# Optimization experiments

Hardware: AMD Instinct MI355X
Metric: run time of the kernel (lower is better)

The kernel has to match this reference:

```python
import jax, jax.numpy as jnp
import numpy as np

E = 8        # num experts
K = 2        # top-k
H = 1024     # hidden size
F = 3584     # intermediate (ffn) size
B, S = 1, 2048


def setup_inputs() -> dict:
    key = jax.random.key(0)
    ks = jax.random.split(key, 5)
    scale_h = 1.0 / np.sqrt(H)
    scale_f = 1.0 / np.sqrt(F)
    return {
        "hidden_states": jax.random.normal(ks[0], (B, S, H), jnp.float32),
        "gate_w": jax.random.normal(ks[1], (E, H), jnp.float32) * scale_h,  # Linear [out,in]
        "w1": jax.random.normal(ks[2], (E, F, H), jnp.float32) * scale_h,
        "w3": jax.random.normal(ks[3], (E, F, H), jnp.float32) * scale_h,
        "w2": jax.random.normal(ks[4], (E, H, F), jnp.float32) * scale_f,
    }


def reference(hidden_states, gate_w, w1, w3, w2):
    b, s, h = hidden_states.shape
    x = hidden_states.reshape(-1, h)                       # [T,H]
    T = x.shape[0]
    # Router: softmax over experts, top-k, renormalize
    router_logits = x @ gate_w.T                           # [T,E]
    routing_weights = jax.nn.softmax(router_logits.astype(jnp.float32), axis=-1)
    topk_w, topk_idx = jax.lax.top_k(routing_weights, K)   # [T,K]
    topk_w = topk_w / jnp.sum(topk_w, axis=-1, keepdims=True)
    # Per-token, per-expert combine weight (0 for unselected experts) --
    # matches the original mask-and-sum over all experts.
    tok = jnp.arange(T)
    expert_weights = jnp.zeros((T, E), jnp.float32).at[tok[:, None], topk_idx].add(topk_w)  # [T,E]
    # Dense per-expert SiLU-gated MLP over all tokens (as the reference loop does),
    # vectorized across experts.
    g = jnp.einsum("th,efh->etf", x, w1)                   # [E,T,F]
    u = jnp.einsum("th,efh->etf", x, w3)                   # [E,T,F]
    act = jax.nn.silu(g) * u                               # [E,T,F]
    y = jnp.einsum("etf,ehf->eth", act, w2)                # [E,T,H]
    out = jnp.einsum("eth,te->th", y, expert_weights.astype(y.dtype))  # [T,H]
    return out.reshape(b, s, h)
```

## Files before the change

kernel.cpp:

```cpp
#include <hip/hip_runtime.h>
#include <hip/hip_bf16.h>

#define T_TOK 2048
#define HID   1024
#define FF    3584
#define NE    8
#define TOPK  2
#define GRIDY 24

typedef __bf16 bf16x8 __attribute__((ext_vector_type(8)));
typedef float  f32x4  __attribute__((ext_vector_type(4)));

#define WS_COUNTS   0u
#define WS_OFFSETS  64u
#define WS_TILECNT  128u
#define WS_TLE      256u
#define WS_TLM      512u
#define WS_TOPKI    4096u
#define WS_TOPKW    20480u
#define WS_SLOTPOS  36864u
#define WS_SLOTROW  53248u
#define WS_ROUTETOK 69632u
#define WS_XG       131072u
#define WS_ACT      (WS_XG + 4096u*1024u*2u)
#define WS_Y        (WS_ACT + 4096u*3584u*2u)
#define Y_STRIDE    (4096u*1024u)

static __device__ __forceinline__ unsigned short f2bf(float f) {
    unsigned int u = __builtin_bit_cast(unsigned int, f);
    u += 0x7FFFu + ((u >> 16) & 1u);
    return (unsigned short)(u >> 16);
}
static __device__ __forceinline__ unsigned int pack2(float a, float b) {
    unsigned int ua = __builtin_bit_cast(unsigned int, a) + 0x8000u;
    unsigned int ub = __builtin_bit_cast(unsigned int, b) + 0x8000u;
    return (ua >> 16) | (ub & 0xFFFF0000u);
}
static __device__ __forceinline__ void gl_lds16(const void* g, void* l) {
    __builtin_amdgcn_global_load_lds((const __attribute__((address_space(1))) unsigned int*)g,
                                     (__attribute__((address_space(3))) unsigned int*)l, 16, 0, 0);
}

__global__ __launch_bounds__(256) void k_router(
    const float* __restrict__ x, const float* __restrict__ gw,
    int* __restrict__ counts, int* __restrict__ topki,
    float* __restrict__ topkw, int* __restrict__ slotpos)
{
    int t = blockIdx.x * 4 + (threadIdx.x >> 6);
    int l = threadIdx.x & 63;
    const float* xr = x + (size_t)t * HID;
    float acc[NE];
#pragma unroll
    for (int e = 0; e < NE; ++e) acc[e] = 0.f;
#pragma unroll
    for (int i = 0; i < 4; ++i) {
        int h = l * 4 + i * 256;
        float4 xv = *(const float4*)(xr + h);
#pragma unroll
        for (int e = 0; e < NE; ++e) {
            float4 g = *(const float4*)(gw + e * HID + h);
            acc[e] += xv.x * g.x + xv.y * g.y + xv.z * g.z + xv.w * g.w;
        }
    }
#pragma unroll
    for (int e = 0; e < NE; ++e) {
#pragma unroll
        for (int off = 32; off; off >>= 1) acc[e] += __shfl_xor(acc[e], off);
    }
    if (l == 0) {
        float best = -1e30f, second = -1e30f;
        int bi = 0, si = 0;
#pragma unroll
        for (int e = 0; e < NE; ++e) {
            float v = acc[e];
            if (v > best) { second = best; si = bi; best = v; bi = e; }
            else if (v > second) { second = v; si = e; }
        }
        float w0 = 1.f / (1.f + __expf(second - best));
        float w1 = 1.f - w0;
        topki[2 * t] = bi;  topki[2 * t + 1] = si;
        topkw[2 * t] = w0;  topkw[2 * t + 1] = w1;
        slotpos[2 * t]     = atomicAdd(&counts[bi], 1);
        slotpos[2 * t + 1] = atomicAdd(&counts[si], 1);
    }
}

__global__ void k_prefix(const int* __restrict__ counts, int* __restrict__ offsets,
                         int* __restrict__ tle, int* __restrict__ tlm,
                         int* __restrict__ tilecnt) {
    if (threadIdx.x == 0) {
        int o = 0;
#pragma unroll
        for (int e = 0; e < NE; ++e) { offsets[e] = o; o += counts[e]; }
        int n = 0;
        for (int e = 0; e < NE; ++e) {
            int t = (counts[e] + 255) >> 8;
            for (int i = 0; i < t; ++i) { tle[n] = e; tlm[n] = i; ++n; }
        }
        tilecnt[0] = n;
    }
}

__global__ void k_fill(const int* __restrict__ topki, const int* __restrict__ slotpos,
                       const int* __restrict__ offsets, int* __restrict__ routetok,
                       int* __restrict__ slotrow) {
    int j = blockIdx.x * blockDim.x + threadIdx.x;
    if (j >= T_TOK * TOPK) return;
    int e = topki[j];
    int row = offsets[e] + slotpos[j];
    routetok[row] = j >> 1;
    slotrow[j] = row;
}

__global__ void k_gather(const float* __restrict__ x, const int* __restrict__ routetok,
                         unsigned short* __restrict__ xg) {
    int j = blockIdx.x * blockDim.x + threadIdx.x;
    int r = j >> 8;
    int c = (j & 255) * 4;
    int tok = routetok[r];
    float4 v = *(const float4*)(x + (size_t)tok * HID + c);
    ushort4 o;
    o.x = f2bf(v.x); o.y = f2bf(v.y); o.z = f2bf(v.z); o.w = f2bf(v.w);
    int sc = c ^ ((r & 7) << 3);
    *(ushort4*)(xg + (size_t)r * HID + sc) = o;
}

__global__ __launch_bounds__(256, 2) void k_gemm1(
    const unsigned short* __restrict__ xg, const float* __restrict__ w1,
    const float* __restrict__ w3, const int* __restrict__ counts,
    const int* __restrict__ offsets, const int* __restrict__ tle,
    const int* __restrict__ tlm, const int* __restrict__ tilecnt,
    unsigned short* __restrict__ act)
{
    int by = blockIdx.y;
    if (by >= tilecnt[0]) return;
    int e = tle[by];
    int rbase = tlm[by] * 256;
    int cnt = counts[e], obase = offsets[e];
    int fbase = blockIdx.x * 64;

    __shared__ __align__(16) unsigned short lA[2][256 * 64];
    __shared__ __align__(16) unsigned short lB1[64 * 64];
    __shared__ __align__(16) unsigned short lB3[64 * 64];

    int tid = threadIdx.x;
    int lane = tid & 63, wv = tid >> 6;
    int wr = wv >> 1, wc = wv & 1;

    const unsigned short* asrc[8];
#pragma unroll
    for (int j = 0; j < 8; ++j) {
        int r = rbase + (tid >> 3) + 32 * j;
        int rg = obase + (r < cnt ? r : (cnt - 1));
        asrc[j] = xg + (size_t)rg * HID + (tid & 7) * 8;
    }
    unsigned short* adst = &lA[0][0] + tid * 8;

    int rb = tid & 63;
    int swzW = (rb & 7) << 3;
    const float* pb1 = w1 + ((size_t)e * FF + fbase + rb) * HID + wv * 16;
    const float* pb3 = w3 + ((size_t)e * FF + fbase + rb) * HID + wv * 16;
    unsigned short* wb1a = lB1 + rb * 64 + ((wv * 16) ^ swzW);
    unsigned short* wb1b = lB1 + rb * 64 + ((wv * 16 + 8) ^ swzW);
    unsigned short* wb3a = lB3 + rb * 64 + ((wv * 16) ^ swzW);
    unsigned short* wb3b = lB3 + rb * 64 + ((wv * 16 + 8) ^ swzW);

    int swzA = (((obase & 7) + (lane & 7)) & 7) << 3;
    int swzB = (lane & 7) << 3;
    int klane = (lane >> 4) * 8;

    f32x4 accg[8][2], accu[8][2];
#pragma unroll
    for (int m = 0; m < 8; ++m)
#pragma unroll
        for (int n = 0; n < 2; ++n) {
            accg[m][n] = (f32x4){0.f, 0.f, 0.f, 0.f};
            accu[m][n] = (f32x4){0.f, 0.f, 0.f, 0.f};
        }

#pragma unroll
    for (int j = 0; j < 8; ++j) gl_lds16(asrc[j], adst + 32 * j * 64);
    float4 r1[4], r3[4];
#pragma unroll
    for (int j = 0; j < 4; ++j) {
        r1[j] = *(const float4*)(pb1 + 4 * j);
        r3[j] = *(const float4*)(pb3 + 4 * j);
    }

    for (int kt = 0; kt < HID / 64; ++kt) {
        int cur = kt & 1;
        if (kt < HID / 64 - 1) {
            unsigned short* nd = &lA[cur ^ 1][0] + tid * 8;
#pragma unroll
            for (int j = 0; j < 8; ++j) gl_lds16(asrc[j] + (kt + 1) * 64, nd + 32 * j * 64);
        }
        {
            uint4 q;
            q.x = pack2(r1[0].x, r1[0].y); q.y = pack2(r1[0].z, r1[0].w);
            q.z = pack2(r1[1].x, r1[1].y); q.w = pack2(r1[1].z, r1[1].w);
            *(uint4*)wb1a = q;
            q.x = pack2(r1[2].x, r1[2].y); q.y = pack2(r1[2].z, r1[2].w);
            q.z = pack2(r1[3].x, r1[3].y); q.w = pack2(r1[3].z, r1[3].w);
            *(uint4*)wb1b = q;
            q.x = pack2(r3[0].x, r3[0].y); q.y = pack2(r3[0].z, r3[0].w);
            q.z = pack2(r3[1].x, r3[1].y); q.w = pack2(r3[1].z, r3[1].w);
            *(uint4*)wb3a = q;
            q.x = pack2(r3[2].x, r3[2].y); q.y = pack2(r3[2].z, r3[2].w);
            q.z = pack2(r3[3].x, r3[3].y); q.w = pack2(r3[3].z, r3[3].w);
            *(uint4*)wb3b = q;
        }
        if (kt < HID / 64 - 1) {
            int kof = (kt + 1) * 64;
#pragma unroll
            for (int j = 0; j < 4; ++j) {
                r1[j] = *(const float4*)(pb1 + kof + 4 * j);
                r3[j] = *(const float4*)(pb3 + kof + 4 * j);
            }
        }
        asm volatile("s_waitcnt lgkmcnt(0)" ::: "memory");
        __builtin_amdgcn_s_barrier();
        __builtin_amdgcn_sched_barrier(0);
        const unsigned short* A = &lA[cur][0];
#pragma unroll
        for (int kk = 0; kk < 2; ++kk) {
            int kc = kk * 32 + klane;
            int kA = kc ^ swzA, kB = kc ^ swzB;
            bf16x8 b1f[2], b3f[2];
#pragma unroll
            for (int n = 0; n < 2; ++n) {
                b1f[n] = *(const bf16x8*)(lB1 + (wc * 32 + n * 16 + (lane & 15)) * 64 + kB);
                b3f[n] = *(const bf16x8*)(lB3 + (wc * 32 + n * 16 + (lane & 15)) * 64 + kB);
            }
#pragma unroll
            for (int m = 0; m < 8; ++m) {
                bf16x8 a = *(const bf16x8*)(A + (wr * 128 + m * 16 + (lane & 15)) * 64 + kA);
#pragma unroll
                for (int n = 0; n < 2; ++n) {
                    accg[m][n] = __builtin_amdgcn_mfma_f32_16x16x32_bf16(a, b1f[n], accg[m][n], 0, 0, 0);
                    accu[m][n] = __builtin_amdgcn_mfma_f32_16x16x32_bf16(a, b3f[n], accu[m][n], 0, 0, 0);
                }
            }
        }
        __builtin_amdgcn_sched_barrier(0);
        asm volatile("s_waitcnt lgkmcnt(0)" ::: "memory");
        __builtin_amdgcn_s_barrier();
    }

#pragma unroll
    for (int m = 0; m < 8; ++m)
#pragma unroll
        for (int n = 0; n < 2; ++n)
#pragma unroll
            for (int r = 0; r < 4; ++r) {
                int lr = wr * 128 + m * 16 + (lane >> 4) * 4 + r;
                if (rbase + lr < cnt) {
                    float g = accg[m][n][r], u = accu[m][n][r];
                    float s = g / (1.f + __expf(-g));
                    int row = obase + rbase + lr;
                    int col = fbase + wc * 32 + n * 16 + (lane & 15);
                    int scol = col ^ ((row & 7) << 3);
                    act[(size_t)row * FF + scol] = f2bf(s * u);
                }
            }
}

__global__ __launch_bounds__(256, 2) void k_gemm2(
    const unsigned short* __restrict__ act, const float* __restrict__ w2,
    const int* __restrict__ counts, const int* __restrict__ offsets,
    const int* __restrict__ tle, const int* __restrict__ tlm,
    const int* __restrict__ tilecnt, float* __restrict__ y, int ks)
{
    int by = blockIdx.y;
    if (by >= tilecnt[0]) return;
    int e = tle[by];
    int rbase = tlm[by] * 256;
    int cnt = counts[e], obase = offsets[e];
    int hbase = blockIdx.x * 128;
    int z = blockIdx.z;
    const int KTOT = FF / 64;
    int per = (KTOT + ks - 1) / ks;
    int kt0 = z * per;
    int ktn = min(KTOT, kt0 + per) - kt0;

    __shared__ __align__(16) unsigned short lA[2][256 * 64];
    __shared__ __align__(16) unsigned short lB[128 * 64];

    int tid = threadIdx.x;
    int lane = tid & 63, wv = tid >> 6;
    int wr = wv >> 1, wc = wv & 1;

    const unsigned short* asrc[8];
#pragma unroll
    for (int j = 0; j < 8; ++j) {
        int r = rbase + (tid >> 3) + 32 * j;
        int rg = obase + (r < cnt ? r : (cnt - 1));
        asrc[j] = act + (size_t)rg * FF + kt0 * 64 + (tid & 7) * 8;
    }
    unsigned short* adst = &lA[0][0] + tid * 8;

    int hr = tid & 127, kh = tid >> 7;
    int swzW = (hr & 7) << 3;
    const float* pb = w2 + ((size_t)e * HID + hbase + hr) * FF + kt0 * 64 + kh * 32;
    unsigned short* wb[4];
#pragma unroll
    for (int j = 0; j < 4; ++j)
        wb[j] = lB + hr * 64 + ((kh * 32 + j * 8) ^ swzW);

    int swzA = (((obase & 7) + (lane & 7)) & 7) << 3;
    int swzB = (lane & 7) << 3;
    int klane = (lane >> 4) * 8;

    f32x4 acc[8][4];
#pragma unroll
    for (int m = 0; m < 8; ++m)
#pragma unroll
        for (int n = 0; n < 4; ++n) acc[m][n] = (f32x4){0.f, 0.f, 0.f, 0.f};

#pragma unroll
    for (int j = 0; j < 8; ++j) gl_lds16(asrc[j], adst + 32 * j * 64);
    float4 rw[8];
#pragma unroll
    for (int j = 0; j < 8; ++j) rw[j] = *(const float4*)(pb + 4 * j);

    for (int kt = 0; kt < ktn; ++kt) {
        int cur = kt & 1;
        if (kt < ktn - 1) {
            unsigned short* nd = &lA[cur ^ 1][0] + tid * 8;
#pragma unroll
            for (int j = 0; j < 8; ++j) gl_lds16(asrc[j] + (kt + 1) * 64, nd + 32 * j * 64);
        }
        {
            uint4 q;
#pragma unroll
            for (int j = 0; j < 4; ++j) {
                q.x = pack2(rw[2 * j].x, rw[2 * j].y);
                q.y = pack2(rw[2 * j].z, rw[2 * j].w);
                q.z = pack2(rw[2 * j + 1].x, rw[2 * j + 1].y);
                q.w = pack2(rw[2 * j + 1].z, rw[2 * j + 1].w);
                *(uint4*)wb[j] = q;
            }
        }
        if (kt < ktn - 1) {
            int kof = (kt + 1) * 64;
#pragma unroll
            for (int j = 0; j < 8; ++j) rw[j] = *(const float4*)(pb + kof + 4 * j);
        }
        asm volatile("s_waitcnt lgkmcnt(0)" ::: "memory");
        __builtin_amdgcn_s_barrier();
        __builtin_amdgcn_sched_barrier(0);
        const unsigned short* A = &lA[cur][0];
#pragma unroll
        for (int kk = 0; kk < 2; ++kk) {
            int kc = kk * 32 + klane;
            int kA = kc ^ swzA, kB = kc ^ swzB;
            bf16x8 bf[4];
#pragma unroll
            for (int n = 0; n < 4; ++n)
                bf[n] = *(const bf16x8*)(lB + (wc * 64 + n * 16 + (lane & 15)) * 64 + kB);
#pragma unroll
            for (int m = 0; m < 8; ++m) {
                bf16x8 a = *(const bf16x8*)(A + (wr * 128 + m * 16 + (lane & 15)) * 64 + kA);
#pragma unroll
                for (int n = 0; n < 4; ++n)
                    acc[m][n] = __builtin_amdgcn_mfma_f32_16x16x32_bf16(a, bf[n], acc[m][n], 0, 0, 0);
            }
        }
        __builtin_amdgcn_sched_barrier(0);
        asm volatile("s_waitcnt lgkmcnt(0)" ::: "memory");
        __builtin_amdgcn_s_barrier();
    }

    float* yz = y + (size_t)z * Y_STRIDE;
#pragma unroll
    for (int m = 0; m < 8; ++m)
#pragma unroll
        for (int n = 0; n < 4; ++n)
#pragma unroll
            for (int r = 0; r < 4; ++r) {
                int lr = wr * 128 + m * 16 + (lane >> 4) * 4 + r;
                if (rbase + lr < cnt) {
                    int col = hbase + wc * 64 + n * 16 + (lane & 15);
                    yz[(size_t)(obase + rbase + lr) * HID + col] = acc[m][n][r];
                }
            }
}

__global__ void k_combine(const float* __restrict__ y, const int* __restrict__ slotrow,
                          const float* __restrict__ topkw, float* __restrict__ out, int ks) {
    int j = blockIdx.x * blockDim.x + threadIdx.x;
    int t = j >> 8, c = j & 255;
    int r0 = slotrow[2 * t], r1 = slotrow[2 * t + 1];
    float w0 = topkw[2 * t], w1 = topkw[2 * t + 1];
    float4 a = {0.f, 0.f, 0.f, 0.f}, b = {0.f, 0.f, 0.f, 0.f};
    for (int z = 0; z < ks; ++z) {
        const float4* yz = (const float4*)(y + (size_t)z * Y_STRIDE);
        float4 av = yz[(size_t)r0 * 256 + c];
        float4 bv = yz[(size_t)r1 * 256 + c];
        a.x += av.x; a.y += av.y; a.z += av.z; a.w += av.w;
        b.x += bv.x; b.y += bv.y; b.z += bv.z; b.w += bv.w;
    }
    float4 o;
    o.x = w0 * a.x + w1 * b.x;
    o.y = w0 * a.y + w1 * b.y;
    o.z = w0 * a.z + w1 * b.z;
    o.w = w0 * a.w + w1 * b.w;
    ((float4*)out)[j] = o;
}

extern "C" void kernel_launch(void* const* d_in, const int* in_sizes, int n_in,
                              void* d_out, int out_size, void* d_ws, size_t ws_size,
                              hipStream_t stream) {
    const float* x  = (const float*)d_in[0];
    const float* gw = (const float*)d_in[1];
    const float* w1 = (const float*)d_in[2];
    const float* w3 = (const float*)d_in[3];
    const float* w2 = (const float*)d_in[4];
    float* out = (float*)d_out;

    char* ws = (char*)d_ws;
    int*   counts   = (int*)(ws + WS_COUNTS);
    int*   offsets  = (int*)(ws + WS_OFFSETS);
    int*   tilecnt  = (int*)(ws + WS_TILECNT);
    int*   tle      = (int*)(ws + WS_TLE);
    int*   tlm      = (int*)(ws + WS_TLM);
    int*   topki    = (int*)(ws + WS_TOPKI);
    float* topkw    = (float*)(ws + WS_TOPKW);
    int*   slotpos  = (int*)(ws + WS_SLOTPOS);
    int*   slotrow  = (int*)(ws + WS_SLOTROW);
    int*   routetok = (int*)(ws + WS_ROUTETOK);
    unsigned short* xg   = (unsigned short*)(ws + WS_XG);
    unsigned short* actb = (unsigned short*)(ws + WS_ACT);
    float* yb = (float*)(ws + WS_Y);

    size_t ybytes = (size_t)Y_STRIDE * 4;
    int ks = 1;
    if (ws_size >= (size_t)WS_Y + 3 * ybytes) ks = 3;
    else if (ws_size >= (size_t)WS_Y + 2 * ybytes) ks = 2;

    hipMemsetAsync(counts, 0, 64, stream);
    k_router<<<T_TOK / 4, 256, 0, stream>>>(x, gw, counts, topki, topkw, slotpos);
    k_prefix<<<1, 64, 0, stream>>>(counts, offsets, tle, tlm, tilecnt);
    k_fill<<<16, 256, 0, stream>>>(topki, slotpos, offsets, routetok, slotrow);
    k_gather<<<4096, 256, 0, stream>>>(x, routetok, xg);
    k_gemm1<<<dim3(FF / 64, GRIDY, 1), 256, 0, stream>>>(xg, w1, w3, counts, offsets, tle, tlm, tilecnt, actb);
    k_gemm2<<<dim3(HID / 128, GRIDY, ks), 256, 0, stream>>>(actb, w2, counts, offsets, tle, tlm, tilecnt, yb, ks);
    k_combine<<<2048, 256, 0, stream>>>(yb, slotrow, topkw, out, ks);
}
```

Before: 322.3 us.

## Shrink MoE GEMM row tiles to 128, drop A double-buffering, use hardware bf16 pack

Halves the per-expert row tile from 256 to 128 in both grouped GEMMs and raises the tile grid bound from 24 to 40, giving more blocks and less padding waste. The double-buffered A prefetch and its hand-placed waitcnt/barrier scheduling are replaced by a single LDS buffer loaded each k-step under plain __syncthreads. The software fp32-to-bf16 rounding is replaced with the v_cvt_pk_bf16_f32 instruction. In exchange, each weight tile is reused across half as many rows, so weight traffic roughly doubles, and the A loads are no longer overlapped with compute.

```diff
diff --git a/kernel.cpp b/kernel.cpp
--- a/kernel.cpp
+++ b/kernel.cpp
@@ -6,7 +6,7 @@
 #define FF    3584
 #define NE    8
 #define TOPK  2
-#define GRIDY 24
+#define GRIDY 40
 
 typedef __bf16 bf16x8 __attribute__((ext_vector_type(8)));
 typedef float  f32x4  __attribute__((ext_vector_type(4)));
@@ -31,10 +31,10 @@
     u += 0x7FFFu + ((u >> 16) & 1u);
     return (unsigned short)(u >> 16);
 }
-static __device__ __forceinline__ unsigned int pack2(float a, float b) {
-    unsigned int ua = __builtin_bit_cast(unsigned int, a) + 0x8000u;
-    unsigned int ub = __builtin_bit_cast(unsigned int, b) + 0x8000u;
-    return (ua >> 16) | (ub & 0xFFFF0000u);
+static __device__ __forceinline__ unsigned int cvtpk(float lo, float hi) {
+    unsigned int r;
+    asm("v_cvt_pk_bf16_f32 %0, %1, %2" : "=v"(r) : "v"(lo), "v"(hi));
+    return r;
 }
 static __device__ __forceinline__ void gl_lds16(const void* g, void* l) {
     __builtin_amdgcn_global_load_lds((const __attribute__((address_space(1))) unsigned int*)g,
@@ -94,7 +94,7 @@
         for (int e = 0; e < NE; ++e) { offsets[e] = o; o += counts[e]; }
         int n = 0;
         for (int e = 0; e < NE; ++e) {
-            int t = (counts[e] + 255) >> 8;
+            int t = (counts[e] + 127) >> 7;
             for (int i = 0; i < t; ++i) { tle[n] = e; tlm[n] = i; ++n; }
         }
         tilecnt[0] = n;
@@ -135,11 +135,11 @@
     int by = blockIdx.y;
     if (by >= tilecnt[0]) return;
     int e = tle[by];
-    int rbase = tlm[by] * 256;
+    int rbase = tlm[by] * 128;
     int cnt = counts[e], obase = offsets[e];
     int fbase = blockIdx.x * 64;
 
-    __shared__ __align__(16) unsigned short lA[2][256 * 64];
+    __shared__ __align__(16) unsigned short lA[128 * 64];
     __shared__ __align__(16) unsigned short lB1[64 * 64];
     __shared__ __align__(16) unsigned short lB3[64 * 64];
 
@@ -147,39 +147,37 @@
     int lane = tid & 63, wv = tid >> 6;
     int wr = wv >> 1, wc = wv & 1;
 
-    const unsigned short* asrc[8];
-#pragma unroll
-    for (int j = 0; j < 8; ++j) {
+    const unsigned short* asrc[4];
+#pragma unroll
+    for (int j = 0; j < 4; ++j) {
         int r = rbase + (tid >> 3) + 32 * j;
-        int rg = obase + (r < cnt ? r : (cnt - 1));
+        int rg = obase + (r < cnt ? r : cnt - 1);
         asrc[j] = xg + (size_t)rg * HID + (tid & 7) * 8;
     }
-    unsigned short* adst = &lA[0][0] + tid * 8;
-
-    int rb = tid & 63;
+    unsigned short* adst = lA + tid * 8;
+
+    int rb = tid & 63, kq = tid >> 6;
     int swzW = (rb & 7) << 3;
-    const float* pb1 = w1 + ((size_t)e * FF + fbase + rb) * HID + wv * 16;
-    const float* pb3 = w3 + ((size_t)e * FF + fbase + rb) * HID + wv * 16;
-    unsigned short* wb1a = lB1 + rb * 64 + ((wv * 16) ^ swzW);
-    unsigned short* wb1b = lB1 + rb * 64 + ((wv * 16 + 8) ^ swzW);
-    unsigned short* wb3a = lB3 + rb * 64 + ((wv * 16) ^ swzW);
-    unsigned short* wb3b = lB3 + rb * 64 + ((wv * 16 + 8) ^ swzW);
+    const float* pb1 = w1 + ((size_t)e * FF + fbase + rb) * HID + kq * 16;
+    const float* pb3 = w3 + ((size_t)e * FF + fbase + rb) * HID + kq * 16;
+    unsigned short* wb1[2] = { lB1 + rb * 64 + ((kq * 16) ^ swzW),
+                               lB1 + rb * 64 + ((kq * 16 + 8) ^ swzW) };
+    unsigned short* wb3[2] = { lB3 + rb * 64 + ((kq * 16) ^ swzW),
+                               lB3 + rb * 64 + ((kq * 16 + 8) ^ swzW) };
 
     int swzA = (((obase & 7) + (lane & 7)) & 7) << 3;
     int swzB = (lane & 7) << 3;
     int klane = (lane >> 4) * 8;
 
-    f32x4 accg[8][2], accu[8][2];
-#pragma unroll
-    for (int m = 0; m < 8; ++m)
+    f32x4 accg[4][2], accu[4][2];
+#pragma unroll
+    for (int m = 0; m < 4; ++m)
 #pragma unroll
         for (int n = 0; n < 2; ++n) {
             accg[m][n] = (f32x4){0.f, 0.f, 0.f, 0.f};
             accu[m][n] = (f32x4){0.f, 0.f, 0.f, 0.f};
         }
 
-#pragma unroll
-    for (int j = 0; j < 8; ++j) gl_lds16(asrc[j], adst + 32 * j * 64);
     float4 r1[4], r3[4];
 #pragma unroll
     for (int j = 0; j < 4; ++j) {
@@ -188,27 +186,24 @@
     }
 
     for (int kt = 0; kt < HID / 64; ++kt) {
-        int cur = kt & 1;
-        if (kt < HID / 64 - 1) {
-            unsigned short* nd = &lA[cur ^ 1][0] + tid * 8;
-#pragma unroll
-            for (int j = 0; j < 8; ++j) gl_lds16(asrc[j] + (kt + 1) * 64, nd + 32 * j * 64);
-        }
+#pragma unroll
+        for (int j = 0; j < 4; ++j) gl_lds16(asrc[j] + kt * 64, adst + j * 2048);
         {
             uint4 q;
-            q.x = pack2(r1[0].x, r1[0].y); q.y = pack2(r1[0].z, r1[0].w);
-            q.z = pack2(r1[1].x, r1[1].y); q.w = pack2(r1[1].z, r1[1].w);
-            *(uint4*)wb1a = q;
-            q.x = pack2(r1[2].x, r1[2].y); q.y = pack2(r1[2].z, r1[2].w);
-            q.z = pack2(r1[3].x, r1[3].y); q.w = pack2(r1[3].z, r1[3].w);
-            *(uint4*)wb1b = q;
-            q.x = pack2(r3[0].x, r3[0].y); q.y = pack2(r3[0].z, r3[0].w);
-            q.z = pack2(r3[1].x, r3[1].y); q.w = pack2(r3[1].z, r3[1].w);
-            *(uint4*)wb3a = q;
-            q.x = pack2(r3[2].x, r3[2].y); q.y = pack2(r3[2].z, r3[2].w);
-            q.z = pack2(r3[3].x, r3[3].y); q.w = pack2(r3[3].z, r3[3].w);
-            *(uint4*)wb3b = q;
-        }
+            q.x = cvtpk(r1[0].x, r1[0].y); q.y = cvtpk(r1[0].z, r1[0].w);
+            q.z = cvtpk(r1[1].x, r1[1].y); q.w = cvtpk(r1[1].z, r1[1].w);
+            *(uint4*)wb1[0] = q;
+            q.x = cvtpk(r1[2].x, r1[2].y); q.y = cvtpk(r1[2].z, r1[2].w);
+            q.z = cvtpk(r1[3].x, r1[3].y); q.w = cvtpk(r1[3].z, r1[3].w);
+            *(uint4*)wb1[1] = q;
+            q.x = cvtpk(r3[0].x, r3[0].y); q.y = cvtpk(r3[0].z, r3[0].w);
+            q.z = cvtpk(r3[1].x, r3[1].y); q.w = cvtpk(r3[1].z, r3[1].w);
+            *(uint4*)wb3[0] = q;
+            q.x = cvtpk(r3[2].x, r3[2].y); q.y = cvtpk(r3[2].z, r3[2].w);
+            q.z = cvtpk(r3[3].x, r3[3].y); q.w = cvtpk(r3[3].z, r3[3].w);
+            *(uint4*)wb3[1] = q;
+        }
+        __syncthreads();
         if (kt < HID / 64 - 1) {
             int kof = (kt + 1) * 64;
 #pragma unroll
@@ -217,10 +212,6 @@
                 r3[j] = *(const float4*)(pb3 + kof + 4 * j);
             }
         }
-        asm volatile("s_waitcnt lgkmcnt(0)" ::: "memory");
-        __builtin_amdgcn_s_barrier();
-        __builtin_amdgcn_sched_barrier(0);
-        const unsigned short* A = &lA[cur][0];
 #pragma unroll
         for (int kk = 0; kk < 2; ++kk) {
             int kc = kk * 32 + klane;
@@ -232,8 +223,8 @@
                 b3f[n] = *(const bf16x8*)(lB3 + (wc * 32 + n * 16 + (lane & 15)) * 64 + kB);
             }
 #pragma unroll
-            for (int m = 0; m < 8; ++m) {
-                bf16x8 a = *(const bf16x8*)(A + (wr * 128 + m * 16 + (lane & 15)) * 64 + kA);
+            for (int m = 0; m < 4; ++m) {
+                bf16x8 a = *(const bf16x8*)(lA + (wr * 64 + m * 16 + (lane & 15)) * 64 + kA);
 #pragma unroll
                 for (int n = 0; n < 2; ++n) {
                     accg[m][n] = __builtin_amdgcn_mfma_f32_16x16x32_bf16(a, b1f[n], accg[m][n], 0, 0, 0);
@@ -241,18 +232,16 @@
                 }
             }
         }
-        __builtin_amdgcn_sched_barrier(0);
-        asm volatile("s_waitcnt lgkmcnt(0)" ::: "memory");
-        __builtin_amdgcn_s_barrier();
-    }
-
-#pragma unroll
-    for (int m = 0; m < 8; ++m)
+        __syncthreads();
+    }
+
+#pragma unroll
+    for (int m = 0; m < 4; ++m)
 #pragma unroll
         for (int n = 0; n < 2; ++n)
 #pragma unroll
             for (int r = 0; r < 4; ++r) {
-                int lr = wr * 128 + m * 16 + (lane >> 4) * 4 + r;
+                int lr = wr * 64 + m * 16 + (lane >> 4) * 4 + r;
                 if (rbase + lr < cnt) {
                     float g = accg[m][n][r], u = accu[m][n][r];
                     float s = g / (1.f + __expf(-g));
@@ -273,30 +262,30 @@
     int by = blockIdx.y;
     if (by >= tilecnt[0]) return;
     int e = tle[by];
-    int rbase = tlm[by] * 256;
+    int rbase = tlm[by] * 128;
     int cnt = counts[e], obase = offsets[e];
     int hbase = blockIdx.x * 128;
     int z = blockIdx.z;
     const int KTOT = FF / 64;
     int per = (KTOT + ks - 1) / ks;
     int kt0 = z * per;
-    int ktn = min(KTOT, kt0 + per) - kt0;
-
-    __shared__ __align__(16) unsigned short lA[2][256 * 64];
+    int ktn = (KTOT < kt0 + per ? KTOT : kt0 + per) - kt0;
+
+    __shared__ __align__(16) unsigned short lA[128 * 64];
     __shared__ __align__(16) unsigned short lB[128 * 64];
 
     int tid = threadIdx.x;
     int lane = tid & 63, wv = tid >> 6;
     int wr = wv >> 1, wc = wv & 1;
 
-    const unsigned short* asrc[8];
-#pragma unroll
-    for (int j = 0; j < 8; ++j) {
+    const unsigned short* asrc[4];
+#pragma unroll
+    for (int j = 0; j < 4; ++j) {
         int r = rbase + (tid >> 3) + 32 * j;
-        int rg = obase + (r < cnt ? r : (cnt - 1));
+        int rg = obase + (r < cnt ? r : cnt - 1);
         asrc[j] = act + (size_t)rg * FF + kt0 * 64 + (tid & 7) * 8;
     }
-    unsigned short* adst = &lA[0][0] + tid * 8;
+    unsigned short* adst = lA + tid * 8;
 
     int hr = tid & 127, kh = tid >> 7;
     int swzW = (hr & 7) << 3;
@@ -310,45 +299,36 @@
     int swzB = (lane & 7) << 3;
     int klane = (lane >> 4) * 8;
 
-    f32x4 acc[8][4];
-#pragma unroll
-    for (int m = 0; m < 8; ++m)
+    f32x4 acc[4][4];
+#pragma unroll
+    for (int m = 0; m < 4; ++m)
 #pragma unroll
         for (int n = 0; n < 4; ++n) acc[m][n] = (f32x4){0.f, 0.f, 0.f, 0.f};
 
-#pragma unroll
-    for (int j = 0; j < 8; ++j) gl_lds16(asrc[j], adst + 32 * j * 64);
     float4 rw[8];
 #pragma unroll
     for (int j = 0; j < 8; ++j) rw[j] = *(const float4*)(pb + 4 * j);
 
     for (int kt = 0; kt < ktn; ++kt) {
-        int cur = kt & 1;
-        if (kt < ktn - 1) {
-            unsigned short* nd = &lA[cur ^ 1][0] + tid * 8;
-#pragma unroll
-            for (int j = 0; j < 8; ++j) gl_lds16(asrc[j] + (kt + 1) * 64, nd + 32 * j * 64);
-        }
+#pragma unroll
+        for (int j = 0; j < 4; ++j) gl_lds16(asrc[j] + kt * 64, adst + j * 2048);
         {
             uint4 q;
 #pragma unroll
             for (int j = 0; j < 4; ++j) {
-                q.x = pack2(rw[2 * j].x, rw[2 * j].y);
-                q.y = pack2(rw[2 * j].z, rw[2 * j].w);
-                q.z = pack2(rw[2 * j + 1].x, rw[2 * j + 1].y);
-                q.w = pack2(rw[2 * j + 1].z, rw[2 * j + 1].w);
+                q.x = cvtpk(rw[2 * j].x, rw[2 * j].y);
+                q.y = cvtpk(rw[2 * j].z, rw[2 * j].w);
+                q.z = cvtpk(rw[2 * j + 1].x, rw[2 * j + 1].y);
+                q.w = cvtpk(rw[2 * j + 1].z, rw[2 * j + 1].w);
                 *(uint4*)wb[j] = q;
             }
         }
+        __syncthreads();
         if (kt < ktn - 1) {
             int kof = (kt + 1) * 64;
 #pragma unroll
             for (int j = 0; j < 8; ++j) rw[j] = *(const float4*)(pb + kof + 4 * j);
         }
-        asm volatile("s_waitcnt lgkmcnt(0)" ::: "memory");
-        __builtin_amdgcn_s_barrier();
-        __builtin_amdgcn_sched_barrier(0);
-        const unsigned short* A = &lA[cur][0];
 #pragma unroll
         for (int kk = 0; kk < 2; ++kk) {
             int kc = kk * 32 + klane;
@@ -358,26 +338,24 @@
             for (int n = 0; n < 4; ++n)
                 bf[n] = *(const bf16x8*)(lB + (wc * 64 + n * 16 + (lane & 15)) * 64 + kB);
 #pragma unroll
-            for (int m = 0; m < 8; ++m) {
-                bf16x8 a = *(const bf16x8*)(A + (wr * 128 + m * 16 + (lane & 15)) * 64 + kA);
+            for (int m = 0; m < 4; ++m) {
+                bf16x8 a = *(const bf16x8*)(lA + (wr * 64 + m * 16 + (lane & 15)) * 64 + kA);
 #pragma unroll
                 for (int n = 0; n < 4; ++n)
                     acc[m][n] = __builtin_amdgcn_mfma_f32_16x16x32_bf16(a, bf[n], acc[m][n], 0, 0, 0);
             }
         }
-        __builtin_amdgcn_sched_barrier(0);
-        asm volatile("s_waitcnt lgkmcnt(0)" ::: "memory");
-        __builtin_amdgcn_s_barrier();
+        __syncthreads();
     }
 
     float* yz = y + (size_t)z * Y_STRIDE;
 #pragma unroll
-    for (int m = 0; m < 8; ++m)
+    for (int m = 0; m < 4; ++m)
 #pragma unroll
         for (int n = 0; n < 4; ++n)
 #pragma unroll
             for (int r = 0; r < 4; ++r) {
-                int lr = wr * 128 + m * 16 + (lane >> 4) * 4 + r;
+                int lr = wr * 64 + m * 16 + (lane >> 4) * 4 + r;
                 if (rbase + lr < cnt) {
                     int col = hbase + wc * 64 + n * 16 + (lane & 15);
                     yz[(size_t)(obase + rbase + lr) * HID + col] = acc[m][n][r];
```

After: 370.1 us. +14.8%, slower.
